# Kernel optimization log

Measured on AMD Instinct MI355X. Metric: run time of the kernel, lower is better.

Reference implementation:

```python
import jax, jax.numpy as jnp
import numpy as np

W1 = 1.0
W2 = 1.0


def setup_inputs() -> dict:
    key = jax.random.key(0)
    k1, k2 = jax.random.split(key)
    points1 = jax.random.normal(k1, (8, 4096, 3), dtype=jnp.float32)
    points2 = jax.random.normal(k2, (8, 4096, 3), dtype=jnp.float32)
    return {"points1": points1, "points2": points2}


def reference(points1, points2):
    # Pairwise squared L2 distances: [B, N1, N2].
    # (torch code does sqrt(dist)**2 which is mathematically identity for dist>=0.)
    diff = points1[:, :, None, :] - points2[:, None, :, :]  # [B, N1, N2, 3]
    dist = jnp.sum(diff * diff, axis=3)                      # [B, N1, N2]
    dist_min1 = jnp.min(dist, axis=2)  # nearest in points2 for each points1: [B, N1]
    dist_min2 = jnp.min(dist, axis=1)  # nearest in points1 for each points2: [B, N2]
    loss1 = dist_min1.mean(axis=1)     # [B]
    loss2 = dist_min2.mean(axis=1)     # [B]
    loss = W1 * loss1 + W2 * loss2
    return loss.mean()  # each_batch=False
```

## Files before the change

kernel.cpp:

```cpp
#include <hip/hip_runtime.h>
#include <float.h>


typedef float v2f __attribute__((ext_vector_type(2)));

#define NBATCH 8
#define NPTS   4096
#define BLK    256
#define PTS    16
#define NCHUNK 32
#define CHUNK  (NPTS / NCHUNK)
#define PAIRS  (CHUNK / 2)

__global__ __launch_bounds__(BLK)
void chamfer_min_kernel(const float* __restrict__ p1,
                        const float* __restrict__ p2,
                        unsigned int* __restrict__ mins )
{
    __shared__ float4 sXY[PAIRS];
    __shared__ float4 sZW[PAIRS];

    int bid   = blockIdx.x;
    int chunk = bid & (NCHUNK - 1);  bid >>= 5;
    int b     = bid & (NBATCH - 1);  bid >>= 3;
    int dir   = bid;

    const float* A    = dir ? p2 : p1;
    const float* Bpts = dir ? p1 : p2;
    int tid = threadIdx.x;

    if (tid < PAIRS) {
        const float* s = Bpts + ((size_t)b * NPTS + chunk * CHUNK + 2 * tid) * 3;
        float x0 = s[0], y0 = s[1], z0 = s[2];
        float x1 = s[3], y1 = s[4], z1 = s[5];
        sXY[tid] = make_float4(x0, x1, y0, y1);
        sZW[tid] = make_float4(z0, z1,
                               x0 * x0 + y0 * y0 + z0 * z0,
                               x1 * x1 + y1 * y1 + z1 * z1);
    }

    v2f  m2x[PTS], m2y[PTS], m2z[PTS];
    float n1[PTS], best[PTS];
#pragma unroll
    for (int k = 0; k < PTS; ++k) {
        const float* s = A + ((size_t)b * NPTS + tid + k * BLK) * 3;
        float x = s[0], y = s[1], z = s[2];
        float mx = -2.0f * x, my = -2.0f * y, mz = -2.0f * z;
        m2x[k] = (v2f){mx, mx};
        m2y[k] = (v2f){my, my};
        m2z[k] = (v2f){mz, mz};
        n1[k]  = x * x + y * y + z * z;
        best[k] = FLT_MAX;
    }
    __syncthreads();

#pragma unroll 2
    for (int p = 0; p < PAIRS; ++p) {
        float4 xy = sXY[p];
        float4 zw = sZW[p];
        v2f qx = (v2f){xy.x, xy.y};
        v2f qy = (v2f){xy.z, xy.w};
        v2f qz = (v2f){zw.x, zw.y};
        v2f qw = (v2f){zw.z, zw.w};
#pragma unroll
        for (int k = 0; k < PTS; ++k) {
            v2f t = __builtin_elementwise_fma(m2x[k], qx, qw);
            t = __builtin_elementwise_fma(m2y[k], qy, t);
            t = __builtin_elementwise_fma(m2z[k], qz, t);
            best[k] = fminf(fminf(best[k], t.x), t.y);
        }
    }

    unsigned int* marr = mins + ((size_t)dir * NBATCH + b) * NPTS + tid;
#pragma unroll
    for (int k = 0; k < PTS; ++k) {
        float d = fmaxf(best[k] + n1[k], 0.0f);
        atomicMin(&marr[k * BLK], __float_as_uint(d));
    }
}

__global__ __launch_bounds__(256)
void chamfer_reduce1(const float* __restrict__ mins, float* __restrict__ partials)
{
    __shared__ float wave_sums[4];
    int idx = blockIdx.x * 256 + threadIdx.x;
    float4 v = ((const float4*)mins)[idx];
    float s = (v.x + v.y) + (v.z + v.w);
#pragma unroll
    for (int off = 32; off > 0; off >>= 1)
        s += __shfl_down(s, off, 64);
    if ((threadIdx.x & 63) == 0) wave_sums[threadIdx.x >> 6] = s;
    __syncthreads();
    if (threadIdx.x == 0)
        partials[blockIdx.x] = (wave_sums[0] + wave_sums[1]) + (wave_sums[2] + wave_sums[3]);
}

__global__ __launch_bounds__(64)
void chamfer_reduce2(const float* __restrict__ partials, float* __restrict__ out)
{
    float s = partials[threadIdx.x];
#pragma unroll
    for (int off = 32; off > 0; off >>= 1)
        s += __shfl_down(s, off, 64);
    if (threadIdx.x == 0) out[0] = s / (float)(NBATCH * NPTS);
}

extern "C" void kernel_launch(void* const* d_in, const int* in_sizes, int n_in,
                              void* d_out, int out_size, void* d_ws, size_t ws_size,
                              hipStream_t stream) {
    const float* p1 = (const float*)d_in[0];
    const float* p2 = (const float*)d_in[1];
    float* out = (float*)d_out;
    unsigned int* mins = (unsigned int*)d_ws;
    float* partials = (float*)d_ws + 2 * NBATCH * NPTS;

    hipMemsetAsync(d_ws, 0xFF, (size_t)2 * NBATCH * NPTS * sizeof(unsigned int), stream);

    int nblocks = 2 * NBATCH * NCHUNK;
    chamfer_min_kernel<<<nblocks, BLK, 0, stream>>>(p1, p2, mins);
    chamfer_reduce1<<<64, 256, 0, stream>>>((const float*)d_ws, partials);
    chamfer_reduce2<<<1, 64, 0, stream>>>(partials, out);
}
```

Before: 81.13 us.

## Replace atomicMin and memset with per-chunk partial mins reduced in second pass

```diff
diff --git a/kernel.cpp b/kernel.cpp
--- a/kernel.cpp
+++ b/kernel.cpp
@@ -11,11 +11,12 @@
 #define NCHUNK 32
 #define CHUNK  (NPTS / NCHUNK)
 #define PAIRS  (CHUNK / 2)
+#define NDB    (2 * NBATCH)
 
 __global__ __launch_bounds__(BLK)
 void chamfer_min_kernel(const float* __restrict__ p1,
                         const float* __restrict__ p2,
-                        unsigned int* __restrict__ mins )
+                        float* __restrict__ mins2 )
 {
     __shared__ float4 sXY[PAIRS];
     __shared__ float4 sZW[PAIRS];
@@ -42,15 +43,25 @@
     v2f  m2x[PTS], m2y[PTS], m2z[PTS];
     float n1[PTS], best[PTS];
 #pragma unroll
-    for (int k = 0; k < PTS; ++k) {
-        const float* s = A + ((size_t)b * NPTS + tid + k * BLK) * 3;
-        float x = s[0], y = s[1], z = s[2];
-        float mx = -2.0f * x, my = -2.0f * y, mz = -2.0f * z;
-        m2x[k] = (v2f){mx, mx};
-        m2y[k] = (v2f){my, my};
-        m2z[k] = (v2f){mz, mz};
-        n1[k]  = x * x + y * y + z * z;
-        best[k] = FLT_MAX;
+    for (int k = 0; k < 4; ++k) {
+        const float* s = A + ((size_t)b * NPTS + k * 1024 + 4 * tid) * 3;
+        float4 f0 = ((const float4*)s)[0];
+        float4 f1 = ((const float4*)s)[1];
+        float4 f2 = ((const float4*)s)[2];
+        float px[4] = {f0.x, f0.w, f1.z, f2.y};
+        float py[4] = {f0.y, f1.x, f1.w, f2.z};
+        float pz[4] = {f0.z, f1.y, f2.x, f2.w};
+#pragma unroll
+        for (int j = 0; j < 4; ++j) {
+            int kk = k * 4 + j;
+            float x = px[j], y = py[j], z = pz[j];
+            float mx = -2.0f * x, my = -2.0f * y, mz = -2.0f * z;
+            m2x[kk] = (v2f){mx, mx};
+            m2y[kk] = (v2f){my, my};
+            m2z[kk] = (v2f){mz, mz};
+            n1[kk]  = x * x + y * y + z * z;
+            best[kk] = FLT_MAX;
+        }
     }
     __syncthreads();
 
@@ -71,21 +82,36 @@
         }
     }
 
-    unsigned int* marr = mins + ((size_t)dir * NBATCH + b) * NPTS + tid;
+    float* slot = mins2 + (((size_t)(dir * NBATCH + b) * NCHUNK + chunk) * NPTS) + 4 * tid;
 #pragma unroll
-    for (int k = 0; k < PTS; ++k) {
-        float d = fmaxf(best[k] + n1[k], 0.0f);
-        atomicMin(&marr[k * BLK], __float_as_uint(d));
+    for (int k = 0; k < 4; ++k) {
+        float4 dv;
+        dv.x = fmaxf(best[k * 4 + 0] + n1[k * 4 + 0], 0.0f);
+        dv.y = fmaxf(best[k * 4 + 1] + n1[k * 4 + 1], 0.0f);
+        dv.z = fmaxf(best[k * 4 + 2] + n1[k * 4 + 2], 0.0f);
+        dv.w = fmaxf(best[k * 4 + 3] + n1[k * 4 + 3], 0.0f);
+        ((float4*)(slot + (size_t)k * 1024))[0] = dv;
     }
 }
 
 __global__ __launch_bounds__(256)
-void chamfer_reduce1(const float* __restrict__ mins, float* __restrict__ partials)
+void chamfer_reduce1(const float* __restrict__ mins2, float* __restrict__ partials)
 {
     __shared__ float wave_sums[4];
-    int idx = blockIdx.x * 256 + threadIdx.x;
-    float4 v = ((const float4*)mins)[idx];
-    float s = (v.x + v.y) + (v.z + v.w);
+    int db = blockIdx.x >> 2;
+    int q  = blockIdx.x & 3;
+    const float4* base = (const float4*)mins2 + ((size_t)db * (NCHUNK * NPTS / 4) + q * 256) + threadIdx.x;
+
+    float4 m = base[0];
+#pragma unroll
+    for (int c = 1; c < NCHUNK; ++c) {
+        float4 v = base[(size_t)c * (NPTS / 4)];
+        m.x = fminf(m.x, v.x);
+        m.y = fminf(m.y, v.y);
+        m.z = fminf(m.z, v.z);
+        m.w = fminf(m.w, v.w);
+    }
+    float s = (m.x + m.y) + (m.z + m.w);
 #pragma unroll
     for (int off = 32; off > 0; off >>= 1)
         s += __shfl_down(s, off, 64);
@@ -111,13 +137,11 @@
     const float* p1 = (const float*)d_in[0];
     const float* p2 = (const float*)d_in[1];
     float* out = (float*)d_out;
-    unsigned int* mins = (unsigned int*)d_ws;
-    float* partials = (float*)d_ws + 2 * NBATCH * NPTS;
+    float* mins2 = (float*)d_ws;
+    float* partials = mins2 + (size_t)NDB * NCHUNK * NPTS;
 
-    hipMemsetAsync(d_ws, 0xFF, (size_t)2 * NBATCH * NPTS * sizeof(unsigned int), stream);
-
-    int nblocks = 2 * NBATCH * NCHUNK;
-    chamfer_min_kernel<<<nblocks, BLK, 0, stream>>>(p1, p2, mins);
-    chamfer_reduce1<<<64, 256, 0, stream>>>((const float*)d_ws, partials);
+    int nblocks = NDB * NCHUNK;
+    chamfer_min_kernel<<<nblocks, BLK, 0, stream>>>(p1, p2, mins2);
+    chamfer_reduce1<<<64, 256, 0, stream>>>(mins2, partials);
     chamfer_reduce2<<<1, 64, 0, stream>>>(partials, out);
 }
```

Result: no change. 80.62 us (-0.6%).
